# Kernel optimization log

Measured on AMD Instinct MI355X. Metric: run time of the kernel, lower is better.

## Reference

```python
import jax, jax.numpy as jnp
import numpy as np

MAX_LORAS, OUT, IN = 8, 4096, 4096
B, S = 4, 2048


def setup_inputs() -> dict:
    key = jax.random.key(0)
    k1, k2, k3 = jax.random.split(key, 3)
    x = jax.random.normal(k1, (B, S, IN), dtype=jnp.float32)
    weight = jax.random.normal(k2, (MAX_LORAS, OUT, IN), dtype=jnp.float32) * 0.02
    adapter_ids = jax.random.randint(k3, (B,), 0, MAX_LORAS, dtype=jnp.int32)
    return {"x": x, "weight": weight, "adapter_ids": adapter_ids}


def reference(x, weight, adapter_ids):
    # Gather a full [OUT, IN] matrix per batch element (matches weight[adapter_ids]).
    w = weight[adapter_ids]                 # [B, OUT, IN]
    # F.linear(x, w) == x @ w^T, batched over B: [B, S, IN] x [B, OUT, IN] -> [B, S, OUT]
    return jnp.einsum('bsi,boi->bso', x, w)
```

## Files before the change

kernel.cpp:

```cpp
#include <hip/hip_runtime.h>
#include <hip/hip_bf16.h>


#define SEQ    2048
#define IN_K   4096
#define OUT_N  4096
#define NB     4

typedef __attribute__((ext_vector_type(8))) short  short8;
typedef __attribute__((ext_vector_type(4))) float  float4v;

constexpr int BM = 256, BN = 256, BK = 64;
constexpr int GT = 512;
constexpr int KT = IN_K / BK;
constexpr int CH = 128 * 64;

__device__ inline short f2b(float f) {
    union { float f; unsigned u; } v; v.f = f;
    unsigned r = v.u + 0x7FFFu + ((v.u >> 16) & 1u);
    return (short)(r >> 16);
}
__device__ inline short8 pack8(float4v lo, float4v hi) {
    short8 r;
    r[0] = f2b(lo[0]); r[1] = f2b(lo[1]); r[2] = f2b(lo[2]); r[3] = f2b(lo[3]);
    r[4] = f2b(hi[0]); r[5] = f2b(hi[1]); r[6] = f2b(hi[2]); r[7] = f2b(hi[3]);
    return r;
}

typedef const __attribute__((address_space(1))) void* gp1_t;
typedef __attribute__((address_space(3))) void*       lp3_t;
__device__ inline void gload_lds16(const void* g, void* l) {
    __builtin_amdgcn_global_load_lds((gp1_t)g, (lp3_t)l, 16, 0, 0);
}

#define WAITV(N)  asm volatile("s_waitcnt vmcnt(" #N ")" ::: "memory")
#define WAITL0()  asm volatile("s_waitcnt lgkmcnt(0)" ::: "memory")
#define BAR()     __builtin_amdgcn_s_barrier()

__global__ __launch_bounds__(256)
void cvt_x_kernel(const float* __restrict__ x, short* __restrict__ o, int n8)
{
    int i = blockIdx.x * blockDim.x + threadIdx.x;
    const int stride = gridDim.x * blockDim.x;
    for (; i < n8; i += stride) {
        const float4v a = *(const float4v*)(x + (size_t)i * 8);
        const float4v b = *(const float4v*)(x + (size_t)i * 8 + 4);
        *(short8*)(o + (size_t)i * 8) = pack8(a, b);
    }
}

__global__ __launch_bounds__(256)
void cvt_w_kernel(const float* __restrict__ w, const int* __restrict__ ids,
                  short* __restrict__ o, int by_id)
{
    const int b  = blockIdx.y;
    const int id = ids[b];
    int slot = b;
    if (by_id) {
        for (int j = 0; j < b; ++j) if (ids[j] == id) return;
        slot = id;
    }
    const float* __restrict__ src = w + (size_t)id   * OUT_N * IN_K;
    short* __restrict__       dst = o + (size_t)slot * OUT_N * IN_K;
    const int n8 = OUT_N * IN_K / 8;
    int i = blockIdx.x * blockDim.x + threadIdx.x;
    const int stride = gridDim.x * blockDim.x;
    for (; i < n8; i += stride) {
        const float4v a = *(const float4v*)(src + (size_t)i * 8);
        const float4v c = *(const float4v*)(src + (size_t)i * 8 + 4);
        *(short8*)(dst + (size_t)i * 8) = pack8(a, c);
    }
}

__global__ __launch_bounds__(GT, 2)
void mll_gemm_v10(const short* __restrict__ A, const short* __restrict__ W,
                  const int* __restrict__ ids, int by_id, float* __restrict__ out)
{
    __shared__ __align__(16) short lds[2][4][CH];

    const int tid  = threadIdx.x;
    const int lane = tid & 63;
    const int wid  = tid >> 6;
    const int wr   = wid >> 2;
    const int wc   = wid & 3;

    const int bid = blockIdx.x;
    const int n   = (bid & 7) * 64 + (bid >> 3);
    const int bx  = n & 15;
    const int by  = (n >> 4) & 7;
    const int bz  = n >> 7;
    const int brow = by * BM, bcol = bx * BN;

    const int wslot = by_id ? ids[bz] : bz;
    const short* __restrict__ Ab = A + (size_t)bz * SEQ * IN_K + (size_t)brow * IN_K;
    const short* __restrict__ Bb = W + (size_t)wslot * OUT_N * IN_K + (size_t)bcol * IN_K;

    const short* gA[2][2];
    const short* gB[2][2];
    int ldso[2];
#pragma unroll
    for (int r = 0; r < 2; ++r) {
        const int c   = tid + r * GT;
        const int row = c >> 3;
        const int sg  = (c & 7) ^ (row & 7);
        ldso[r] = c * 8;
        gA[0][r] = Ab + (size_t)row         * IN_K + sg * 8;
        gA[1][r] = Ab + (size_t)(128 + row) * IN_K + sg * 8;
        gB[0][r] = Bb + (size_t)row         * IN_K + sg * 8;
        gB[1][r] = Bb + (size_t)(128 + row) * IN_K + sg * 8;
    }

#define STAGE_A(h, t) do { short* d_ = &lds[(t) & 1][h][0];                    \
        gload_lds16(gA[h][0] + (t) * BK, d_ + ldso[0]);                        \
        gload_lds16(gA[h][1] + (t) * BK, d_ + ldso[1]); } while (0)
#define STAGE_B(h, t) do { short* d_ = &lds[(t) & 1][2 + (h)][0];              \
        gload_lds16(gB[h][0] + (t) * BK, d_ + ldso[0]);                        \
        gload_lds16(gB[h][1] + (t) * BK, d_ + ldso[1]); } while (0)

    float4v acc[8][4];
#pragma unroll
    for (int m = 0; m < 8; ++m)
#pragma unroll
        for (int q = 0; q < 4; ++q)
            acc[m][q] = (float4v){0.f, 0.f, 0.f, 0.f};

    const int lr  = lane & 15;
    const int ksl = lane >> 4;
    const int sw  = lr & 7;
    const int so0 = ((0 + ksl) ^ sw) * 8;
    const int so1 = ((4 + ksl) ^ sw) * 8;

    const int cA = wr;
    const int cB = 2 + (wc >> 1);
    const int bRow0 = ((wc & 1) * 64 + lr) * BK;

    short8 fA[4][2], fBlo[2][2], fBhi[2][2];

    STAGE_A(0, 0); STAGE_A(1, 0); STAGE_B(0, 0); STAGE_B(1, 0);
    STAGE_A(0, 1); STAGE_A(1, 1); STAGE_B(0, 1); STAGE_B(1, 1);
    WAITV(8);
    BAR();

    for (int t = 0; t < KT; ++t) {
        const short* sA = &lds[t & 1][cA][0];
        const short* sB = &lds[t & 1][cB][0];

#pragma unroll
        for (int m = 0; m < 4; ++m) {
            fA[m][0] = *(const short8*)(sA + (m * 16 + lr) * BK + so0);
            fA[m][1] = *(const short8*)(sA + (m * 16 + lr) * BK + so1);
        }
#pragma unroll
        for (int q = 0; q < 2; ++q) {
            fBlo[q][0] = *(const short8*)(sB + bRow0 + q * 16 * BK + so0);
            fBlo[q][1] = *(const short8*)(sB + bRow0 + q * 16 * BK + so1);
        }
        if (t >= 1 && t + 1 < KT) STAGE_A(0, t + 1);
        BAR(); WAITL0();
        __builtin_amdgcn_s_setprio(1);
#pragma unroll
        for (int m = 0; m < 4; ++m)
#pragma unroll
            for (int q = 0; q < 2; ++q) {
                acc[m][q] = __builtin_amdgcn_mfma_f32_16x16x32_bf16(
                    fA[m][0], fBlo[q][0], acc[m][q], 0, 0, 0);
                acc[m][q] = __builtin_amdgcn_mfma_f32_16x16x32_bf16(
                    fA[m][1], fBlo[q][1], acc[m][q], 0, 0, 0);
            }
        __builtin_amdgcn_s_setprio(0);
        BAR();

#pragma unroll
        for (int q = 0; q < 2; ++q) {
            fBhi[q][0] = *(const short8*)(sB + bRow0 + (q + 2) * 16 * BK + so0);
            fBhi[q][1] = *(const short8*)(sB + bRow0 + (q + 2) * 16 * BK + so1);
        }
        if (t >= 1 && t + 1 < KT) STAGE_A(1, t + 1);
        BAR(); WAITL0();
        __builtin_amdgcn_s_setprio(1);
#pragma unroll
        for (int m = 0; m < 4; ++m)
#pragma unroll
            for (int q = 0; q < 2; ++q) {
                acc[m][q + 2] = __builtin_amdgcn_mfma_f32_16x16x32_bf16(
                    fA[m][0], fBhi[q][0], acc[m][q + 2], 0, 0, 0);
                acc[m][q + 2] = __builtin_amdgcn_mfma_f32_16x16x32_bf16(
                    fA[m][1], fBhi[q][1], acc[m][q + 2], 0, 0, 0);
            }
        __builtin_amdgcn_s_setprio(0);
        BAR();

#pragma unroll
        for (int m = 0; m < 4; ++m) {
            fA[m][0] = *(const short8*)(sA + ((m + 4) * 16 + lr) * BK + so0);
            fA[m][1] = *(const short8*)(sA + ((m + 4) * 16 + lr) * BK + so1);
        }
        if (t + 2 < KT) STAGE_B(0, t + 2);
        BAR(); WAITL0();
        __builtin_amdgcn_s_setprio(1);
#pragma unroll
        for (int m = 0; m < 4; ++m)
#pragma unroll
            for (int q = 0; q < 2; ++q) {
                acc[m + 4][q + 2] = __builtin_amdgcn_mfma_f32_16x16x32_bf16(
                    fA[m][0], fBhi[q][0], acc[m + 4][q + 2], 0, 0, 0);
                acc[m + 4][q + 2] = __builtin_amdgcn_mfma_f32_16x16x32_bf16(
                    fA[m][1], fBhi[q][1], acc[m + 4][q + 2], 0, 0, 0);
            }
        __builtin_amdgcn_s_setprio(0);
        BAR();

        if (t + 2 < KT) STAGE_B(1, t + 2);
        if (t <= KT - 3)      WAITV(4);
        else if (t == KT - 2) WAITV(0);
        BAR();
        __builtin_amdgcn_s_setprio(1);
#pragma unroll
        for (int m = 0; m < 4; ++m)
#pragma unroll
            for (int q = 0; q < 2; ++q) {
                acc[m + 4][q] = __builtin_amdgcn_mfma_f32_16x16x32_bf16(
                    fA[m][0], fBlo[q][0], acc[m + 4][q], 0, 0, 0);
                acc[m + 4][q] = __builtin_amdgcn_mfma_f32_16x16x32_bf16(
                    fA[m][1], fBlo[q][1], acc[m + 4][q], 0, 0, 0);
            }
        __builtin_amdgcn_s_setprio(0);
        BAR();
    }

    float* __restrict__ ob = out + (size_t)bz * SEQ * OUT_N;
    const int lrow = ksl * 4;
#pragma unroll
    for (int m = 0; m < 8; ++m) {
#pragma unroll
        for (int q = 0; q < 4; ++q) {
            const int r0 = brow + wr * 128 + m * 16 + lrow;
            const int c  = bcol + wc * 64 + q * 16 + lr;
#pragma unroll
            for (int j = 0; j < 4; ++j)
                ob[(size_t)(r0 + j) * OUT_N + c] = acc[m][q][j];
        }
    }
#undef STAGE_A
#undef STAGE_B
}

__device__ inline int xr(int row) { return (row & 3) ^ ((row >> 2) & 3); }

__global__ __launch_bounds__(256, 2)
void mll_gemm_fused(const float* __restrict__ x,
                    const float* __restrict__ w,
                    const int*   __restrict__ adapter_ids,
                    float* __restrict__ out)
{
    constexpr int FBM = 128, FBN = 128, FBK = 32;
    __shared__ __align__(16) short As[2][FBM * FBK];
    __shared__ __align__(16) short Bs[2][FBN * FBK];

    const int tid  = threadIdx.x;
    const int lane = tid & 63;
    const int wave = tid >> 6;
    const int wr   = wave >> 1;
    const int wc   = wave & 1;

    const int b    = blockIdx.z;
    const int aid  = adapter_ids[b];
    const int brow = blockIdx.y * FBM;
    const int bcol = blockIdx.x * FBN;

    const float* __restrict__ xb = x + (size_t)b   * SEQ   * IN_K;
    const float* __restrict__ wb = w + (size_t)aid * OUT_N * IN_K;

    float4v ra[2][2], rb[2][2];

    auto LOADG = [&](int kt) {
        const int k0 = kt * FBK;
#pragma unroll
        for (int g = 0; g < 2; ++g) {
            const int f  = tid + g * 256;
            const int r  = f >> 2;
            const int sl = f & 3;
            const float* pa = xb + (size_t)(brow + r) * IN_K + k0 + sl * 8;
            ra[g][0] = *(const float4v*)pa;
            ra[g][1] = *(const float4v*)(pa + 4);
            const float* pb = wb + (size_t)(bcol + r) * IN_K + k0 + sl * 8;
            rb[g][0] = *(const float4v*)pb;
            rb[g][1] = *(const float4v*)(pb + 4);
        }
    };
    auto STORE_LDS = [&](int buf) {
#pragma unroll
        for (int g = 0; g < 2; ++g) {
            const int f  = tid + g * 256;
            const int r  = f >> 2;
            const int sl = f & 3;
            const int ss = sl ^ xr(r);
            *(short8*)&As[buf][r * FBK + ss * 8] = pack8(ra[g][0], ra[g][1]);
            *(short8*)&Bs[buf][r * FBK + ss * 8] = pack8(rb[g][0], rb[g][1]);
        }
    };

    float4v acc[4][4];
#pragma unroll
    for (int m = 0; m < 4; ++m)
#pragma unroll
        for (int q = 0; q < 4; ++q)
            acc[m][q] = (float4v){0.f, 0.f, 0.f, 0.f};

    const int NT = IN_K / FBK;
    LOADG(0); STORE_LDS(0); __syncthreads();
    int cur = 0;
    for (int kt = 0; kt < NT; ++kt) {
        if (kt + 1 < NT) LOADG(kt + 1);
        short8 af[4], bfr[4];
        const int ksl = lane >> 4;
#pragma unroll
        for (int m = 0; m < 4; ++m) {
            const int rrk = wr * 64 + m * 16 + (lane & 15);
            af[m] = *(const short8*)&As[cur][rrk * FBK + (ksl ^ xr(rrk)) * 8];
        }
#pragma unroll
        for (int q = 0; q < 4; ++q) {
            const int rc = wc * 64 + q * 16 + (lane & 15);
            bfr[q] = *(const short8*)&Bs[cur][rc * FBK + (ksl ^ xr(rc)) * 8];
        }
#pragma unroll
        for (int m = 0; m < 4; ++m)
#pragma unroll
            for (int q = 0; q < 4; ++q)
                acc[m][q] = __builtin_amdgcn_mfma_f32_16x16x32_bf16(
                    af[m], bfr[q], acc[m][q], 0, 0, 0);
        if (kt + 1 < NT) STORE_LDS(cur ^ 1);
        __syncthreads();
        cur ^= 1;
    }

    float* __restrict__ ob = out + (size_t)b * SEQ * OUT_N;
    const int lrow = (lane >> 4) * 4;
    const int lcol = lane & 15;
#pragma unroll
    for (int m = 0; m < 4; ++m) {
#pragma unroll
        for (int q = 0; q < 4; ++q) {
            const int r0 = brow + wr * 64 + m * 16 + lrow;
            const int c  = bcol + wc * 64 + q * 16 + lcol;
#pragma unroll
            for (int j = 0; j < 4; ++j)
                ob[(size_t)(r0 + j) * OUT_N + c] = acc[m][q][j];
        }
    }
}

extern "C" void kernel_launch(void* const* d_in, const int* in_sizes, int n_in,
                              void* d_out, int out_size, void* d_ws, size_t ws_size,
                              hipStream_t stream)
{
    const float* x   = (const float*)d_in[0];
    const float* w   = (const float*)d_in[1];
    const int*   ids = (const int*)d_in[2];
    float* out = (float*)d_out;

    const size_t xb_bytes  = (size_t)NB * SEQ   * IN_K * sizeof(short);
    const size_t wb4_bytes = (size_t)NB * OUT_N * IN_K * sizeof(short);
    const size_t wb8_bytes = (size_t)8  * OUT_N * IN_K * sizeof(short);

    if (ws_size >= xb_bytes + wb8_bytes) {
        short* xb16 = (short*)d_ws;
        short* wb16 = (short*)((char*)d_ws + xb_bytes);
        cvt_x_kernel<<<2048, 256, 0, stream>>>(x, xb16, NB * SEQ * IN_K / 8);
        cvt_w_kernel<<<dim3(1024, NB), 256, 0, stream>>>(w, ids, wb16, 1);
        mll_gemm_v10<<<512, GT, 0, stream>>>(xb16, wb16, ids, 1, out);
    } else if (ws_size >= xb_bytes + wb4_bytes) {
        short* xb16 = (short*)d_ws;
        short* wb16 = (short*)((char*)d_ws + xb_bytes);
        cvt_x_kernel<<<2048, 256, 0, stream>>>(x, xb16, NB * SEQ * IN_K / 8);
        cvt_w_kernel<<<dim3(1024, NB), 256, 0, stream>>>(w, ids, wb16, 0);
        mll_gemm_v10<<<512, GT, 0, stream>>>(xb16, wb16, ids, 0, out);
    } else {
        mll_gemm_fused<<<dim3(OUT_N / 128, SEQ / 128, NB), 256, 0, stream>>>(
            x, w, ids, out);
    }
}
```

Baseline: 331.8 us.

## Merge conversion kernels into one launch and drop redundant GEMM barriers

```diff
diff --git a/kernel.cpp b/kernel.cpp
--- a/kernel.cpp
+++ b/kernel.cpp
@@ -34,46 +34,46 @@
 }
 
 #define WAITV(N)  asm volatile("s_waitcnt vmcnt(" #N ")" ::: "memory")
-#define WAITL0()  asm volatile("s_waitcnt lgkmcnt(0)" ::: "memory")
+#define WAITL(N)  asm volatile("s_waitcnt lgkmcnt(" #N ")" ::: "memory")
 #define BAR()     __builtin_amdgcn_s_barrier()
 
 __global__ __launch_bounds__(256)
-void cvt_x_kernel(const float* __restrict__ x, short* __restrict__ o, int n8)
+void cvt_all_kernel(const float* __restrict__ x, const float* __restrict__ w,
+                    const int* __restrict__ ids, short* __restrict__ xo,
+                    short* __restrict__ wo, int by_id)
 {
-    int i = blockIdx.x * blockDim.x + threadIdx.x;
+    const int y = blockIdx.y;
     const int stride = gridDim.x * blockDim.x;
-    for (; i < n8; i += stride) {
-        const float4v a = *(const float4v*)(x + (size_t)i * 8);
-        const float4v b = *(const float4v*)(x + (size_t)i * 8 + 4);
-        *(short8*)(o + (size_t)i * 8) = pack8(a, b);
-    }
-}
-
-__global__ __launch_bounds__(256)
-void cvt_w_kernel(const float* __restrict__ w, const int* __restrict__ ids,
-                  short* __restrict__ o, int by_id)
-{
-    const int b  = blockIdx.y;
-    const int id = ids[b];
-    int slot = b;
-    if (by_id) {
-        for (int j = 0; j < b; ++j) if (ids[j] == id) return;
-        slot = id;
-    }
-    const float* __restrict__ src = w + (size_t)id   * OUT_N * IN_K;
-    short* __restrict__       dst = o + (size_t)slot * OUT_N * IN_K;
-    const int n8 = OUT_N * IN_K / 8;
-    int i = blockIdx.x * blockDim.x + threadIdx.x;
-    const int stride = gridDim.x * blockDim.x;
-    for (; i < n8; i += stride) {
-        const float4v a = *(const float4v*)(src + (size_t)i * 8);
-        const float4v c = *(const float4v*)(src + (size_t)i * 8 + 4);
-        *(short8*)(dst + (size_t)i * 8) = pack8(a, c);
+    if (y < NB) {
+        const int id = ids[y];
+        int slot = y;
+        if (by_id) {
+            for (int j = 0; j < y; ++j) if (ids[j] == id) return;
+            slot = id;
+        }
+        const float* __restrict__ src = w + (size_t)id   * OUT_N * IN_K;
+        short* __restrict__       dst = wo + (size_t)slot * OUT_N * IN_K;
+        const int n8 = OUT_N * IN_K / 8;
+        for (int i = blockIdx.x * blockDim.x + threadIdx.x; i < n8; i += stride) {
+            const float4v a = *(const float4v*)(src + (size_t)i * 8);
+            const float4v c = *(const float4v*)(src + (size_t)i * 8 + 4);
+            *(short8*)(dst + (size_t)i * 8) = pack8(a, c);
+        }
+    } else {
+        const int half = y - NB;
+        const int n8h  = NB * SEQ * IN_K / 16;
+        const float* __restrict__ src = x  + (size_t)half * n8h * 8;
+        short* __restrict__       dst = xo + (size_t)half * n8h * 8;
+        for (int i = blockIdx.x * blockDim.x + threadIdx.x; i < n8h; i += stride) {
+            const float4v a = *(const float4v*)(src + (size_t)i * 8);
+            const float4v c = *(const float4v*)(src + (size_t)i * 8 + 4);
+            *(short8*)(dst + (size_t)i * 8) = pack8(a, c);
+        }
     }
 }
 
 __global__ __launch_bounds__(GT, 2)
-void mll_gemm_v10(const short* __restrict__ A, const short* __restrict__ W,
+void mll_gemm_v11(const short* __restrict__ A, const short* __restrict__ W,
                   const int* __restrict__ ids, int by_id, float* __restrict__ out)
 {
     __shared__ __align__(16) short lds[2][4][CH];
@@ -156,7 +156,8 @@
             fBlo[q][1] = *(const short8*)(sB + bRow0 + q * 16 * BK + so1);
         }
         if (t >= 1 && t + 1 < KT) STAGE_A(0, t + 1);
-        BAR(); WAITL0();
+        WAITL(8);
+        BAR(); WAITL(0);
         __builtin_amdgcn_s_setprio(1);
 #pragma unroll
         for (int m = 0; m < 4; ++m)
@@ -168,7 +169,6 @@
                     fA[m][1], fBlo[q][1], acc[m][q], 0, 0, 0);
             }
         __builtin_amdgcn_s_setprio(0);
-        BAR();
 
 #pragma unroll
         for (int q = 0; q < 2; ++q) {
@@ -176,7 +176,7 @@
             fBhi[q][1] = *(const short8*)(sB + bRow0 + (q + 2) * 16 * BK + so1);
         }
         if (t >= 1 && t + 1 < KT) STAGE_A(1, t + 1);
-        BAR(); WAITL0();
+        BAR(); WAITL(0);
         __builtin_amdgcn_s_setprio(1);
 #pragma unroll
         for (int m = 0; m < 4; ++m)
@@ -196,7 +196,8 @@
             fA[m][1] = *(const short8*)(sA + ((m + 4) * 16 + lr) * BK + so1);
         }
         if (t + 2 < KT) STAGE_B(0, t + 2);
-        BAR(); WAITL0();
+        WAITL(4);
+        BAR(); WAITL(0);
         __builtin_amdgcn_s_setprio(1);
 #pragma unroll
         for (int m = 0; m < 4; ++m)
@@ -208,7 +209,6 @@
                     fA[m][1], fBhi[q][1], acc[m + 4][q + 2], 0, 0, 0);
             }
         __builtin_amdgcn_s_setprio(0);
-        BAR();
 
         if (t + 2 < KT) STAGE_B(1, t + 2);
         if (t <= KT - 3)      WAITV(4);
@@ -225,7 +225,6 @@
                     fA[m][1], fBlo[q][1], acc[m + 4][q], 0, 0, 0);
             }
         __builtin_amdgcn_s_setprio(0);
-        BAR();
     }
 
     float* __restrict__ ob = out + (size_t)bz * SEQ * OUT_N;
@@ -367,15 +366,13 @@
     if (ws_size >= xb_bytes + wb8_bytes) {
         short* xb16 = (short*)d_ws;
         short* wb16 = (short*)((char*)d_ws + xb_bytes);
-        cvt_x_kernel<<<2048, 256, 0, stream>>>(x, xb16, NB * SEQ * IN_K / 8);
-        cvt_w_kernel<<<dim3(1024, NB), 256, 0, stream>>>(w, ids, wb16, 1);
-        mll_gemm_v10<<<512, GT, 0, stream>>>(xb16, wb16, ids, 1, out);
+        cvt_all_kernel<<<dim3(1024, NB + 2), 256, 0, stream>>>(x, w, ids, xb16, wb16, 1);
+        mll_gemm_v11<<<512, GT, 0, stream>>>(xb16, wb16, ids, 1, out);
     } else if (ws_size >= xb_bytes + wb4_bytes) {
         short* xb16 = (short*)d_ws;
         short* wb16 = (short*)((char*)d_ws + xb_bytes);
-        cvt_x_kernel<<<2048, 256, 0, stream>>>(x, xb16, NB * SEQ * IN_K / 8);
-        cvt_w_kernel<<<dim3(1024, NB), 256, 0, stream>>>(w, ids, wb16, 0);
-        mll_gemm_v10<<<512, GT, 0, stream>>>(xb16, wb16, ids, 0, out);
+        cvt_all_kernel<<<dim3(1024, NB + 2), 256, 0, stream>>>(x, w, ids, xb16, wb16, 0);
+        mll_gemm_v11<<<512, GT, 0, stream>>>(xb16, wb16, ids, 0, out);
     } else {
         mll_gemm_fused<<<dim3(OUT_N / 128, SEQ / 128, NB), 256, 0, stream>>>(
             x, w, ids, out);
```

Result: faster. 322.7 us (-2.7%).
